# Kernel tuning notes

Measured on AMD Instinct MI355X. Metric: run time of the kernel, lower is better.

## Reference

```python
import jax, jax.numpy as jnp
import numpy as np

N, E, B = 20000, 200000, 16
ND, ED, GD, HD, DOF = 64, 32, 32, 128, 6
PI = 3.14159265358979

def _hat(v):
    x, y, z = v[..., 0], v[..., 1], v[..., 2]
    O = jnp.zeros_like(x)
    return jnp.stack([jnp.stack([O, -z, y], -1),
                      jnp.stack([z, O, -x], -1),
                      jnp.stack([-y, x, O], -1)], -2)

def _so3_exp(phi):
    th2 = jnp.sum(phi * phi, -1, keepdims=True)
    th = jnp.sqrt(th2 + 1e-12)
    a = jnp.where(th < 1e-4, 1.0 - th2 / 6.0, jnp.sin(th) / th)
    b = jnp.where(th < 1e-4, 0.5 - th2 / 24.0, (1.0 - jnp.cos(th)) / th2)
    K = _hat(phi)
    I = jnp.eye(3, dtype=phi.dtype)
    return I + a[..., None] * K + b[..., None] * (K @ K)

def _se3_exp(rho, phi):
    # returns (R, t) of Exp([rho, phi]) with rotation part phi
    th2 = jnp.sum(phi * phi, -1, keepdims=True)
    th = jnp.sqrt(th2 + 1e-12)
    a = jnp.where(th < 1e-4, 1.0 - th2 / 6.0, jnp.sin(th) / th)
    b = jnp.where(th < 1e-4, 0.5 - th2 / 24.0, (1.0 - jnp.cos(th)) / th2)
    c = jnp.where(th < 1e-4, 1.0 / 6.0 - th2 / 120.0, (th - jnp.sin(th)) / (th2 * th))
    K = _hat(phi)
    KK = K @ K
    I = jnp.eye(3, dtype=phi.dtype)
    R = I + a[..., None] * K + b[..., None] * KK
    V = I + b[..., None] * K + c[..., None] * KK
    t = jnp.einsum('nij,nj->ni', V, rho)
    return R, t

def _comp(Ra, ta, Rb, tb):
    return Ra @ Rb, jnp.einsum('nij,nj->ni', Ra, tb) + ta

def _inv(R, t):
    Rt = jnp.swapaxes(R, -1, -2)
    return Rt, -jnp.einsum('nij,nj->ni', Rt, t)

def _vec(R, t):
    # flattened [R | t] 3x4 -> 12
    return jnp.concatenate([R, t[..., None]], -1).reshape(R.shape[0], 12)

def setup_inputs() -> dict:
    key = jax.random.key(0)
    ks = jax.random.split(key, 16)
    T_R = _so3_exp(0.5 * jax.random.normal(ks[0], (N, 3)))
    Tij_R = _so3_exp(0.5 * jax.random.normal(ks[1], (E, 3)))
    return {
        'xfeat': jax.random.normal(ks[2], (N, ND), jnp.float32),
        'T_R': T_R.astype(jnp.float32),
        'T_t': jax.random.normal(ks[3], (N, 3), jnp.float32),
        'edge_feat': jax.random.normal(ks[4], (E, ED), jnp.float32),
        'Tij_R': Tij_R.astype(jnp.float32),
        'Tij_t': jax.random.normal(ks[5], (E, 3), jnp.float32),
        'u': jax.random.normal(ks[6], (B, GD), jnp.float32),
        'edge_index': jax.random.randint(ks[7], (2, E), 0, N),
        'batch': jnp.sort(jax.random.randint(ks[8], (N,), 0, B)),
        'W1': 0.05 * jax.random.normal(ks[9], (2 * ND + 12 + ED, HD), jnp.float32),
        'b1': jnp.zeros((HD,), jnp.float32),
        'W2': 0.05 * jax.random.normal(ks[10], (HD, HD), jnp.float32),
        'b2': jnp.zeros((HD,), jnp.float32),
        'W3': 0.05 * jax.random.normal(ks[11], (HD + GD + ND, HD), jnp.float32),
        'b3': jnp.zeros((HD,), jnp.float32),
        'W4': 0.05 * jax.random.normal(ks[12], (HD, ND + DOF), jnp.float32),
        'b4': jnp.zeros((ND + DOF,), jnp.float32),
    }

def reference(xfeat, T_R, T_t, edge_feat, Tij_R, Tij_t, u,
              edge_index, batch, W1, b1, W2, b2, W3, b3, W4, b4):
    n = xfeat.shape[0]
    i, j = edge_index[0], edge_index[1]
    xfi, xfj = xfeat[i], xfeat[j]
    Ri, ti = T_R[i], T_t[i]
    Rj, tj = T_R[j], T_t[j]
    # T_err_ij = Tj * Ti.inv() * Tij_hat.inv()
    Rii, tii = _inv(Ri, ti)
    Ra, ta = _comp(Rj, tj, Rii, tii)
    Rhi, thi = _inv(Tij_R, Tij_t)
    Reij, teij = _comp(Ra, ta, Rhi, thi)
    # T_err_ji = Ti * Tj.inv() * Tij_hat
    Rji_, tji_ = _inv(Rj, tj)
    Rb, tb = _comp(Ri, ti, Rji_, tji_)
    Reji, teji = _comp(Rb, tb, Tij_R, Tij_t)
    f_ij = jnp.concatenate([xfi, xfj, edge_feat, _vec(Reij, teij)], 1)
    f_ji = jnp.concatenate([xfj, xfi, edge_feat, _vec(Reji, teji)], 1)
    feats = jnp.concatenate([f_ij, f_ji], 0)          # [2E, 172]
    j_both = jnp.concatenate([j, i], 0)               # [2E]
    h = jax.nn.relu(feats @ W1 + b1)
    h = jax.nn.relu(h @ W2 + b2)                      # [2E, HD]
    sums = jax.ops.segment_sum(h, j_both, num_segments=n)
    cnt = jax.ops.segment_sum(jnp.ones((h.shape[0], 1), h.dtype), j_both, num_segments=n)
    aggr = sums / jnp.maximum(cnt, 1.0)               # scatter_mean
    g = jnp.concatenate([aggr, xfeat, u[batch]], 1)
    out = jax.nn.relu(g @ W3 + b3) @ W4 + b4
    xupd, tupd = out[:, :-DOF], out[:, -DOF:]
    rho, phi = tupd[:, :3], tupd[:, 3:]
    # SquashRot: bound rotation angle to pi via tanh
    th = jnp.linalg.norm(phi, axis=-1, keepdims=True)
    phi = phi * (PI * jnp.tanh(th / PI) / (th + 1e-8))
    Rd, td = _se3_exp(rho, phi)
    R_out, t_out = _comp(Rd, td, T_R, T_t)            # boxplus_left: Exp(d) * T
    xfeat_out = xfeat + xupd
    theta = jnp.linalg.norm(phi, axis=-1, keepdims=True)
    return jnp.concatenate([xfeat_out, R_out.reshape(n, 9), t_out, theta], -1)
```

## Files before the change

### kernel.cpp

```cpp
#include <hip/hip_runtime.h>
#include <math.h>

#define ND 64
#define ED 32
#define GD 32
#define HD 128
#define DOF 6
#define K1 172
#define K1PAD 192
#define KG 224
#define N4P 80
#define NOUT 70
#define OUTC 77
#define MT 128
#define FP 200
#define TD 32
#define GP 232
#define HP 136
#define OP 84
#define MAXD 96
#define PI_F 3.14159265358979f

typedef short short8 __attribute__((ext_vector_type(8)));
typedef float f32x4  __attribute__((ext_vector_type(4)));

__device__ __forceinline__ unsigned short f2b(float f) {
    unsigned int u = __float_as_uint(f);
    u += 0x7fffu + ((u >> 16) & 1u);
    return (unsigned short)(u >> 16);
}
__device__ __forceinline__ float b2f(unsigned short b) {
    return __uint_as_float(((unsigned int)b) << 16);
}

__device__ __forceinline__ void mul33_abt(const float* A, const float* B, float* C) {
#pragma unroll
    for (int r = 0; r < 3; r++)
#pragma unroll
        for (int c = 0; c < 3; c++)
            C[3*r+c] = A[3*r+0]*B[3*c+0] + A[3*r+1]*B[3*c+1] + A[3*r+2]*B[3*c+2];
}

__global__ void __launch_bounds__(256)
pack_w(const float* __restrict__ W1, const float* __restrict__ W2,
       const float* __restrict__ W3, const float* __restrict__ W4,
       unsigned short* __restrict__ W1b, unsigned short* __restrict__ W2b,
       unsigned short* __restrict__ W3b, unsigned short* __restrict__ W4b)
{
    int idx = blockIdx.x * 256 + threadIdx.x;
    if (idx < K1PAD * HD) {
        int k = idx >> 7, n = idx & 127;
        float v = (k < K1) ? W1[k * HD + n] : 0.f;
        int kc = k >> 5, kr = k & 31, q = kr >> 3, j = kr & 7;
        W1b[(((kc * 8 + (n >> 4)) * 4 + q) * 16 + (n & 15)) * 8 + j] = f2b(v);
        return;
    }
    idx -= K1PAD * HD;
    if (idx < HD * HD) {
        int k = idx >> 7, n = idx & 127;
        float v = W2[k * HD + n];
        int kc = k >> 5, kr = k & 31, q = kr >> 3, j = kr & 7;
        W2b[(((kc * 8 + (n >> 4)) * 4 + q) * 16 + (n & 15)) * 8 + j] = f2b(v);
        return;
    }
    idx -= HD * HD;
    if (idx < KG * HD) {
        int k = idx >> 7, n = idx & 127;
        int sk = (k < HD) ? ((k & 7) * 16 + (k >> 3)) : k;
        float v = W3[sk * HD + n];
        int kc = k >> 5, kr = k & 31, q = kr >> 3, j = kr & 7;
        W3b[(((kc * 8 + (n >> 4)) * 4 + q) * 16 + (n & 15)) * 8 + j] = f2b(v);
        return;
    }
    idx -= KG * HD;
    if (idx < HD * N4P) {
        int k = idx / N4P, n = idx % N4P;
        float v = (n < NOUT) ? W4[k * NOUT + n] : 0.f;
        int kc = k >> 5, kr = k & 31, q = kr >> 3, j = kr & 7;
        W4b[(((kc * 5 + (n >> 4)) * 4 + q) * 16 + (n & 15)) * 8 + j] = f2b(v);
    }
}

__global__ void __launch_bounds__(256)
build_csr(const int* __restrict__ edge_index, int* __restrict__ cnti,
          int* __restrict__ list, int E)
{
    int d = blockIdx.x * 256 + threadIdx.x;
    if (d >= 2 * E) return;
    const int tgt = (d < E) ? edge_index[E + d] : edge_index[d - E];
    const int slot = atomicAdd(&cnti[tgt], 1);
    if (slot < MAXD) list[(size_t)tgt * MAXD + slot] = d;
}

__global__ void __launch_bounds__(256, 3)
edge_kernel(const float* __restrict__ xfeat, const float* __restrict__ T_R,
            const float* __restrict__ T_t, const float* __restrict__ edge_feat,
            const float* __restrict__ Tij_R, const float* __restrict__ Tij_t,
            const int* __restrict__ edge_index,
            const unsigned short* __restrict__ W1b, const float* __restrict__ b1,
            const unsigned short* __restrict__ W2b, const float* __restrict__ b2,
            unsigned short* __restrict__ hbuf, int E)
{
    __shared__ unsigned short fbuf[MT * FP];
    const int tid = threadIdx.x;
    const int dir0 = blockIdx.x * MT;
    const int ndir = min(MT, 2 * E - dir0);

    {
        const int r = tid >> 1;
        const int half = tid & 1;
        const int drow = dir0 + r;
        int s1 = 0, s2 = 0, er = 0;
        if (r < ndir) {
            const bool fwd = (drow < E);
            er = fwd ? drow : drow - E;
            const int ni = edge_index[er];
            const int nj = edge_index[E + er];
            s1 = fwd ? ni : nj;
            s2 = fwd ? nj : ni;
        }
#pragma unroll
        for (int gg = 0; gg < 20; gg++) {
            const int c4 = (half * 20 + gg) * 4;
            float4 v;
            if (c4 < 64)        v = *(const float4*)&xfeat[s1 * ND + c4];
            else if (c4 < 128)  v = *(const float4*)&xfeat[s2 * ND + (c4 - 64)];
            else                v = *(const float4*)&edge_feat[er * ED + (c4 - 128)];
            ushort4 o; o.x = f2b(v.x); o.y = f2b(v.y); o.z = f2b(v.z); o.w = f2b(v.w);
            *(ushort4*)&fbuf[r * FP + c4] = o;
        }
    }
    if (tid < MT && tid < ndir) {
        const int dir = dir0 + tid;
        const bool fwd = (dir < E);
        const int e = fwd ? dir : dir - E;
        const int ni = edge_index[e];
        const int nj = edge_index[E + e];
        float Ri[9], Rj[9], TR[9], ti[3], tj[3], Tt[3];
#pragma unroll
        for (int q = 0; q < 9; q++) { Ri[q] = T_R[9*ni+q]; Rj[q] = T_R[9*nj+q]; TR[q] = Tij_R[9*e+q]; }
#pragma unroll
        for (int q = 0; q < 3; q++) { ti[q] = T_t[3*ni+q]; tj[q] = T_t[3*nj+q]; Tt[q] = Tij_t[3*e+q]; }
        float A[9];
        mul33_abt(Rj, Ri, A);
        float Re[9], te[3];
        if (fwd) {
            mul33_abt(A, TR, Re);
#pragma unroll
            for (int r = 0; r < 3; r++)
                te[r] = tj[r]
                      - (A[3*r+0]*ti[0] + A[3*r+1]*ti[1] + A[3*r+2]*ti[2])
                      - (Re[3*r+0]*Tt[0] + Re[3*r+1]*Tt[1] + Re[3*r+2]*Tt[2]);
        } else {
#pragma unroll
            for (int r = 0; r < 3; r++)
#pragma unroll
                for (int c = 0; c < 3; c++)
                    Re[3*r+c] = A[r]*TR[c] + A[3+r]*TR[3+c] + A[6+r]*TR[6+c];
            const float d0 = Tt[0]-tj[0], d1 = Tt[1]-tj[1], d2 = Tt[2]-tj[2];
#pragma unroll
            for (int r = 0; r < 3; r++)
                te[r] = ti[r] + A[r]*d0 + A[3+r]*d1 + A[6+r]*d2;
        }
        unsigned short* fr = &fbuf[tid * FP];
#pragma unroll
        for (int r = 0; r < 3; r++) {
            fr[160 + 4*r + 0] = f2b(Re[3*r+0]);
            fr[160 + 4*r + 1] = f2b(Re[3*r+1]);
            fr[160 + 4*r + 2] = f2b(Re[3*r+2]);
            fr[160 + 4*r + 3] = f2b(te[r]);
        }
#pragma unroll
        for (int c = 172; c < K1PAD; c++) fr[c] = 0;
    }
    __syncthreads();

    const int wv = tid >> 6;
    const int lane = tid & 63;
    const int nl = lane & 15;
    const int quad = lane >> 4;
    const int m0w = wv * 32;
    const int laneoff = quad * 128 + nl * 8;

    float bias1[8], bias2[8];
#pragma unroll
    for (int nt = 0; nt < 8; nt++) { bias1[nt] = b1[nt*16 + nl]; bias2[nt] = b2[nt*16 + nl]; }

    f32x4 acc[2][8];
#pragma unroll
    for (int rt = 0; rt < 2; rt++)
#pragma unroll
        for (int nt = 0; nt < 8; nt++) acc[rt][nt] = (f32x4)0.f;

#pragma unroll
    for (int kc = 0; kc < 6; kc++) {
        short8 a0 = *(const short8*)&fbuf[(m0w +  0 + nl) * FP + kc*32 + quad*8];
        short8 a1 = *(const short8*)&fbuf[(m0w + 16 + nl) * FP + kc*32 + quad*8];
#pragma unroll
        for (int nt = 0; nt < 8; nt++) {
            short8 b = *(const short8*)(W1b + (kc*8 + nt)*512 + laneoff);
            acc[0][nt] = __builtin_amdgcn_mfma_f32_16x16x32_bf16(a0, b, acc[0][nt], 0, 0, 0);
            acc[1][nt] = __builtin_amdgcn_mfma_f32_16x16x32_bf16(a1, b, acc[1][nt], 0, 0, 0);
        }
    }
#pragma unroll
    for (int rt = 0; rt < 2; rt++)
#pragma unroll
        for (int nt = 0; nt < 8; nt++) {
            const int col = nt*16 + nl;
#pragma unroll
            for (int r = 0; r < 4; r++) {
                const int row = m0w + rt*16 + quad*4 + r;
                fbuf[row * FP + col] = f2b(fmaxf(acc[rt][nt][r] + bias1[nt], 0.f));
            }
        }

#pragma unroll
    for (int rt = 0; rt < 2; rt++)
#pragma unroll
        for (int nt = 0; nt < 8; nt++) acc[rt][nt] = (f32x4)0.f;
#pragma unroll
    for (int kc = 0; kc < 4; kc++) {
        short8 a0 = *(const short8*)&fbuf[(m0w +  0 + nl) * FP + kc*32 + quad*8];
        short8 a1 = *(const short8*)&fbuf[(m0w + 16 + nl) * FP + kc*32 + quad*8];
#pragma unroll
        for (int nt = 0; nt < 8; nt++) {
            short8 b = *(const short8*)(W2b + (kc*8 + nt)*512 + laneoff);
            acc[0][nt] = __builtin_amdgcn_mfma_f32_16x16x32_bf16(a0, b, acc[0][nt], 0, 0, 0);
            acc[1][nt] = __builtin_amdgcn_mfma_f32_16x16x32_bf16(a1, b, acc[1][nt], 0, 0, 0);
        }
    }

#pragma unroll
    for (int rt = 0; rt < 2; rt++)
#pragma unroll
        for (int r = 0; r < 4; r++) {
            const int m = m0w + rt*16 + quad*4 + r;
            if (m < ndir) {
                short8 hv;
#pragma unroll
                for (int nt = 0; nt < 8; nt++)
                    hv[nt] = (short)f2b(fmaxf(acc[rt][nt][r] + bias2[nt], 0.f));
                *(short8*)(hbuf + (size_t)(dir0 + m) * HD + nl*8) = hv;
            }
        }
}

__global__ void __launch_bounds__(256)
node_kernel(const float* __restrict__ xfeat, const float* __restrict__ T_R,
            const float* __restrict__ T_t, const float* __restrict__ u,
            const int* __restrict__ batch,
            const unsigned short* __restrict__ W3b, const float* __restrict__ b3,
            const unsigned short* __restrict__ W4b, const float* __restrict__ b4,
            const unsigned short* __restrict__ hbuf, const int* __restrict__ list,
            const int* __restrict__ cnti,
            float* __restrict__ out, int Nn)
{
    __shared__ unsigned short gbuf[TD * GP];
    __shared__ unsigned short hid[TD * HP];
    __shared__ float obuf[TD * OP];
    const int tid = threadIdx.x;
    const int wv = tid >> 6, lane = tid & 63;
    const int n0 = blockIdx.x * TD;
    const int nn = min(TD, Nn - n0);

#pragma unroll 2
    for (int i = 0; i < 8; i++) {
        const int d = wv + 4*i;
        if (d < nn) {
            const int n = n0 + d;
            const int deg = cnti[n];
            const int degl = min(deg, MAXD);
            const float inv = 1.0f / (float)max(deg, 1);
            const int* lp = list + (size_t)n * MAXD;
            float a0 = 0.f, a1 = 0.f;
            int k = 0;
            for (; k + 2 <= degl; k += 2) {
                const int e0 = lp[k], e1 = lp[k+1];
                const unsigned int v0 = *(const unsigned int*)(hbuf + (size_t)e0 * HD + 2*lane);
                const unsigned int v1 = *(const unsigned int*)(hbuf + (size_t)e1 * HD + 2*lane);
                a0 += b2f((unsigned short)v0) + b2f((unsigned short)v1);
                a1 += b2f((unsigned short)(v0 >> 16)) + b2f((unsigned short)(v1 >> 16));
            }
            if (k < degl) {
                const unsigned int v0 = *(const unsigned int*)(hbuf + (size_t)lp[k] * HD + 2*lane);
                a0 += b2f((unsigned short)v0);
                a1 += b2f((unsigned short)(v0 >> 16));
            }
            const unsigned int pk = (unsigned int)f2b(a0 * inv) | ((unsigned int)f2b(a1 * inv) << 16);
            *(unsigned int*)&gbuf[d * GP + 2*lane] = pk;
        }
    }
    for (int idx = tid; idx < TD * 24; idx += 256) {
        const int d = idx / 24;
        if (d < nn) {
            const int n = n0 + d;
            const int c4 = (idx % 24) * 4;
            float4 v;
            if (c4 < 64) v = *(const float4*)&xfeat[(size_t)n * ND + c4];
            else         v = *(const float4*)&u[(size_t)batch[n] * GD + (c4 - 64)];
            ushort4 o; o.x = f2b(v.x); o.y = f2b(v.y); o.z = f2b(v.z); o.w = f2b(v.w);
            *(ushort4*)&gbuf[d * GP + 128 + c4] = o;
        }
    }
    __syncthreads();

    const int nl = lane & 15, quad = lane >> 4;
    const int laneoff = quad * 128 + nl * 8;

    f32x4 acc3[2][2];
#pragma unroll
    for (int mt = 0; mt < 2; mt++)
#pragma unroll
        for (int t = 0; t < 2; t++) acc3[mt][t] = (f32x4)0.f;
#pragma unroll
    for (int kc = 0; kc < 7; kc++) {
        short8 A0 = *(const short8*)&gbuf[( 0 + nl) * GP + kc*32 + quad*8];
        short8 A1 = *(const short8*)&gbuf[(16 + nl) * GP + kc*32 + quad*8];
#pragma unroll
        for (int t = 0; t < 2; t++) {
            const int nt = wv*2 + t;
            short8 B = *(const short8*)(W3b + (kc*8 + nt)*512 + laneoff);
            acc3[0][t] = __builtin_amdgcn_mfma_f32_16x16x32_bf16(A0, B, acc3[0][t], 0, 0, 0);
            acc3[1][t] = __builtin_amdgcn_mfma_f32_16x16x32_bf16(A1, B, acc3[1][t], 0, 0, 0);
        }
    }
#pragma unroll
    for (int t = 0; t < 2; t++) {
        const int col = (wv*2 + t)*16 + nl;
        const float bb = b3[col];
#pragma unroll
        for (int mt = 0; mt < 2; mt++)
#pragma unroll
            for (int r = 0; r < 4; r++)
                hid[(mt*16 + quad*4 + r) * HP + col] = f2b(fmaxf(acc3[mt][t][r] + bb, 0.f));
    }
    __syncthreads();

    f32x4 acc4[2][2];
#pragma unroll
    for (int mt = 0; mt < 2; mt++)
#pragma unroll
        for (int t = 0; t < 2; t++) acc4[mt][t] = (f32x4)0.f;
    const int nt1 = (wv == 0) ? 4 : -1;
#pragma unroll
    for (int kc = 0; kc < 4; kc++) {
        short8 A0 = *(const short8*)&hid[( 0 + nl) * HP + kc*32 + quad*8];
        short8 A1 = *(const short8*)&hid[(16 + nl) * HP + kc*32 + quad*8];
        short8 B0 = *(const short8*)(W4b + (kc*5 + wv)*512 + laneoff);
        acc4[0][0] = __builtin_amdgcn_mfma_f32_16x16x32_bf16(A0, B0, acc4[0][0], 0, 0, 0);
        acc4[1][0] = __builtin_amdgcn_mfma_f32_16x16x32_bf16(A1, B0, acc4[1][0], 0, 0, 0);
        if (nt1 >= 0) {
            short8 B1 = *(const short8*)(W4b + (kc*5 + nt1)*512 + laneoff);
            acc4[0][1] = __builtin_amdgcn_mfma_f32_16x16x32_bf16(A0, B1, acc4[0][1], 0, 0, 0);
            acc4[1][1] = __builtin_amdgcn_mfma_f32_16x16x32_bf16(A1, B1, acc4[1][1], 0, 0, 0);
        }
    }
    {
        const int col0 = wv*16 + nl;
        const float bb0 = (col0 < NOUT) ? b4[col0] : 0.f;
#pragma unroll
        for (int mt = 0; mt < 2; mt++)
#pragma unroll
            for (int r = 0; r < 4; r++)
                obuf[(mt*16 + quad*4 + r) * OP + col0] = acc4[mt][0][r] + bb0;
        if (nt1 >= 0) {
            const int col1 = nt1*16 + nl;
            const float bb1 = (col1 < NOUT) ? b4[col1] : 0.f;
#pragma unroll
            for (int mt = 0; mt < 2; mt++)
#pragma unroll
                for (int r = 0; r < 4; r++)
                    obuf[(mt*16 + quad*4 + r) * OP + col1] = acc4[mt][1][r] + bb1;
        }
    }
    __syncthreads();

    for (int idx = tid; idx < TD * ND; idx += 256) {
        const int d = idx >> 6, c = idx & 63;
        if (d < nn) {
            const int n = n0 + d;
            out[(size_t)n * OUTC + c] = xfeat[(size_t)n * ND + c] + obuf[d * OP + c];
        }
    }
    if (tid < nn) {
        const int n = n0 + tid;
        const float r0 = obuf[tid*OP + 64], r1 = obuf[tid*OP + 65], r2 = obuf[tid*OP + 66];
        float p0 = obuf[tid*OP + 67], p1 = obuf[tid*OP + 68], p2 = obuf[tid*OP + 69];
        const float th0 = sqrtf(p0*p0 + p1*p1 + p2*p2);
        const float s = PI_F * tanhf(th0 / PI_F) / (th0 + 1e-8f);
        p0 *= s; p1 *= s; p2 *= s;
        const float pp = p0*p0 + p1*p1 + p2*p2;
        const float th = sqrtf(pp + 1e-12f);
        float a, b, c;
        if (th < 1e-4f) { a = 1.f - pp/6.f; b = 0.5f - pp/24.f; c = 1.f/6.f - pp/120.f; }
        else { const float sn = sinf(th), cs = cosf(th); a = sn/th; b = (1.f-cs)/pp; c = (th-sn)/(pp*th); }
        float Rd[9], V[9];
        Rd[0]=1.f+b*(p0*p0-pp); Rd[1]=-a*p2+b*p0*p1; Rd[2]= a*p1+b*p0*p2;
        Rd[3]= a*p2+b*p1*p0;    Rd[4]=1.f+b*(p1*p1-pp); Rd[5]=-a*p0+b*p1*p2;
        Rd[6]=-a*p1+b*p2*p0;    Rd[7]= a*p0+b*p2*p1;  Rd[8]=1.f+b*(p2*p2-pp);
        V[0]=1.f+c*(p0*p0-pp);  V[1]=-b*p2+c*p0*p1;   V[2]= b*p1+c*p0*p2;
        V[3]= b*p2+c*p1*p0;     V[4]=1.f+c*(p1*p1-pp); V[5]=-b*p0+c*p1*p2;
        V[6]=-b*p1+c*p2*p0;     V[7]= b*p0+c*p2*p1;   V[8]=1.f+c*(p2*p2-pp);
        const float td0 = V[0]*r0 + V[1]*r1 + V[2]*r2;
        const float td1 = V[3]*r0 + V[4]*r1 + V[5]*r2;
        const float td2 = V[6]*r0 + V[7]*r1 + V[8]*r2;
        float TRn[9], Ttn[3];
#pragma unroll
        for (int q = 0; q < 9; q++) TRn[q] = T_R[9*n+q];
#pragma unroll
        for (int q = 0; q < 3; q++) Ttn[q] = T_t[3*n+q];
        float* o = out + (size_t)n * OUTC + 64;
#pragma unroll
        for (int r = 0; r < 3; r++)
#pragma unroll
            for (int cc = 0; cc < 3; cc++)
                o[3*r+cc] = Rd[3*r+0]*TRn[cc] + Rd[3*r+1]*TRn[3+cc] + Rd[3*r+2]*TRn[6+cc];
        o[9]  = Rd[0]*Ttn[0] + Rd[1]*Ttn[1] + Rd[2]*Ttn[2] + td0;
        o[10] = Rd[3]*Ttn[0] + Rd[4]*Ttn[1] + Rd[5]*Ttn[2] + td1;
        o[11] = Rd[6]*Ttn[0] + Rd[7]*Ttn[1] + Rd[8]*Ttn[2] + td2;
        o[12] = sqrtf(pp);
    }
}

extern "C" void kernel_launch(void* const* d_in, const int* in_sizes, int n_in,
                              void* d_out, int out_size, void* d_ws, size_t ws_size,
                              hipStream_t stream)
{
    const float* xfeat     = (const float*)d_in[0];
    const float* T_R       = (const float*)d_in[1];
    const float* T_t       = (const float*)d_in[2];
    const float* edge_feat = (const float*)d_in[3];
    const float* Tij_R     = (const float*)d_in[4];
    const float* Tij_t     = (const float*)d_in[5];
    const float* u         = (const float*)d_in[6];
    const int*   edge_index= (const int*)d_in[7];
    const int*   batch     = (const int*)d_in[8];
    const float* W1 = (const float*)d_in[9],  *b1 = (const float*)d_in[10];
    const float* W2 = (const float*)d_in[11], *b2 = (const float*)d_in[12];
    const float* W3 = (const float*)d_in[13], *b3 = (const float*)d_in[14];
    const float* W4 = (const float*)d_in[15], *b4 = (const float*)d_in[16];
    const int N = in_sizes[0] / ND;
    const int E = in_sizes[3] / ED;

    char* p = (char*)d_ws;
    unsigned short* W1b = (unsigned short*)p;  p += (size_t)K1PAD * HD * 2;
    unsigned short* W2b = (unsigned short*)p;  p += (size_t)HD * HD * 2;
    unsigned short* W3b = (unsigned short*)p;  p += (size_t)KG * HD * 2;
    unsigned short* W4b = (unsigned short*)p;  p += (size_t)HD * N4P * 2;
    unsigned short* hbuf = (unsigned short*)p; p += (size_t)2 * E * HD * 2;
    int* list = (int*)p;                       p += (size_t)N * MAXD * 4;
    int* cnti = (int*)p;

    hipMemsetAsync(cnti, 0, (size_t)N * 4, stream);
    const int packn = K1PAD*HD + HD*HD + KG*HD + HD*N4P;
    pack_w<<<(packn + 255) / 256, 256, 0, stream>>>(W1, W2, W3, W4, W1b, W2b, W3b, W4b);
    build_csr<<<(2 * E + 255) / 256, 256, 0, stream>>>(edge_index, cnti, list, E);

    const int eb = (2 * E + MT - 1) / MT;
    edge_kernel<<<eb, 256, 0, stream>>>(xfeat, T_R, T_t, edge_feat, Tij_R, Tij_t,
                                        edge_index, W1b, b1, W2b, b2, hbuf, E);
    const int nb = (N + TD - 1) / TD;
    node_kernel<<<nb, 256, 0, stream>>>(xfeat, T_R, T_t, u, batch, W3b, b3, W4b, b4,
                                        hbuf, list, cnti, (float*)d_out, N);
}
```

Baseline: 311.7 us.

## Precompute bf16 features and edge poses, load MFMA operands directly from global

```diff
diff --git a/kernel.cpp b/kernel.cpp
--- a/kernel.cpp
+++ b/kernel.cpp
@@ -13,8 +13,8 @@
 #define NOUT 70
 #define OUTC 77
 #define MT 128
-#define FP 200
-#define TD 32
+#define HP1 136
+#define TDN 16
 #define GP 232
 #define HP 136
 #define OP 84
@@ -32,7 +32,6 @@
 __device__ __forceinline__ float b2f(unsigned short b) {
     return __uint_as_float(((unsigned int)b) << 16);
 }
-
 __device__ __forceinline__ void mul33_abt(const float* A, const float* B, float* C) {
 #pragma unroll
     for (int r = 0; r < 3; r++)
@@ -42,10 +41,13 @@
 }
 
 __global__ void __launch_bounds__(256)
-pack_w(const float* __restrict__ W1, const float* __restrict__ W2,
-       const float* __restrict__ W3, const float* __restrict__ W4,
-       unsigned short* __restrict__ W1b, unsigned short* __restrict__ W2b,
-       unsigned short* __restrict__ W3b, unsigned short* __restrict__ W4b)
+prep(const float* __restrict__ W1, const float* __restrict__ W2,
+     const float* __restrict__ W3, const float* __restrict__ W4,
+     const float* __restrict__ xfeat, const float* __restrict__ edge_feat,
+     unsigned short* __restrict__ W1b, unsigned short* __restrict__ W2b,
+     unsigned short* __restrict__ W3b, unsigned short* __restrict__ W4b,
+     unsigned short* __restrict__ xb, unsigned short* __restrict__ eb,
+     int N, int E)
 {
     int idx = blockIdx.x * 256 + threadIdx.x;
     if (idx < K1PAD * HD) {
@@ -58,18 +60,16 @@
     idx -= K1PAD * HD;
     if (idx < HD * HD) {
         int k = idx >> 7, n = idx & 127;
-        float v = W2[k * HD + n];
         int kc = k >> 5, kr = k & 31, q = kr >> 3, j = kr & 7;
-        W2b[(((kc * 8 + (n >> 4)) * 4 + q) * 16 + (n & 15)) * 8 + j] = f2b(v);
+        W2b[(((kc * 8 + (n >> 4)) * 4 + q) * 16 + (n & 15)) * 8 + j] = f2b(W2[k * HD + n]);
         return;
     }
     idx -= HD * HD;
     if (idx < KG * HD) {
         int k = idx >> 7, n = idx & 127;
         int sk = (k < HD) ? ((k & 7) * 16 + (k >> 3)) : k;
-        float v = W3[sk * HD + n];
         int kc = k >> 5, kr = k & 31, q = kr >> 3, j = kr & 7;
-        W3b[(((kc * 8 + (n >> 4)) * 4 + q) * 16 + (n & 15)) * 8 + j] = f2b(v);
+        W3b[(((kc * 8 + (n >> 4)) * 4 + q) * 16 + (n & 15)) * 8 + j] = f2b(W3[sk * HD + n]);
         return;
     }
     idx -= KG * HD;
@@ -78,109 +78,122 @@
         float v = (n < NOUT) ? W4[k * NOUT + n] : 0.f;
         int kc = k >> 5, kr = k & 31, q = kr >> 3, j = kr & 7;
         W4b[(((kc * 5 + (n >> 4)) * 4 + q) * 16 + (n & 15)) * 8 + j] = f2b(v);
+        return;
+    }
+    idx -= HD * N4P;
+    const int nx4 = N * ND / 4;
+    if (idx < nx4) {
+        const float4 v = *(const float4*)&xfeat[idx * 4];
+        ushort4 o; o.x = f2b(v.x); o.y = f2b(v.y); o.z = f2b(v.z); o.w = f2b(v.w);
+        *(ushort4*)&xb[idx * 4] = o;
+        return;
+    }
+    idx -= nx4;
+    if (idx < E * ED / 4) {
+        const float4 v = *(const float4*)&edge_feat[idx * 4];
+        ushort4 o; o.x = f2b(v.x); o.y = f2b(v.y); o.z = f2b(v.z); o.w = f2b(v.w);
+        *(ushort4*)&eb[idx * 4] = o;
     }
 }
 
 __global__ void __launch_bounds__(256)
-build_csr(const int* __restrict__ edge_index, int* __restrict__ cnti,
-          int* __restrict__ list, int E)
+pose_csr(const float* __restrict__ T_R, const float* __restrict__ T_t,
+         const float* __restrict__ Tij_R, const float* __restrict__ Tij_t,
+         const int* __restrict__ edge_index,
+         unsigned short* __restrict__ poseb, int* __restrict__ cnti,
+         int* __restrict__ list, int E)
 {
-    int d = blockIdx.x * 256 + threadIdx.x;
-    if (d >= 2 * E) return;
-    const int tgt = (d < E) ? edge_index[E + d] : edge_index[d - E];
+    const int g = blockIdx.x * 256 + threadIdx.x;
+    if (g >= 2 * E) return;
+    const bool fwd = (g < E);
+    const int e = fwd ? g : g - E;
+    const int ni = edge_index[e];
+    const int nj = edge_index[E + e];
+    const int tgt = fwd ? nj : ni;
     const int slot = atomicAdd(&cnti[tgt], 1);
-    if (slot < MAXD) list[(size_t)tgt * MAXD + slot] = d;
+    if (slot < MAXD) list[(size_t)tgt * MAXD + slot] = g;
+
+    float Ri[9], Rj[9], TR[9], ti[3], tj[3], Tt[3];
+#pragma unroll
+    for (int q = 0; q < 9; q++) { Ri[q] = T_R[9*ni+q]; Rj[q] = T_R[9*nj+q]; TR[q] = Tij_R[9*e+q]; }
+#pragma unroll
+    for (int q = 0; q < 3; q++) { ti[q] = T_t[3*ni+q]; tj[q] = T_t[3*nj+q]; Tt[q] = Tij_t[3*e+q]; }
+    float A[9];
+    mul33_abt(Rj, Ri, A);
+    float Re[9], te[3];
+    if (fwd) {
+        mul33_abt(A, TR, Re);
+#pragma unroll
+        for (int r = 0; r < 3; r++)
+            te[r] = tj[r]
+                  - (A[3*r+0]*ti[0] + A[3*r+1]*ti[1] + A[3*r+2]*ti[2])
+                  - (Re[3*r+0]*Tt[0] + Re[3*r+1]*Tt[1] + Re[3*r+2]*Tt[2]);
+    } else {
+#pragma unroll
+        for (int r = 0; r < 3; r++)
+#pragma unroll
+            for (int c = 0; c < 3; c++)
+                Re[3*r+c] = A[r]*TR[c] + A[3+r]*TR[3+c] + A[6+r]*TR[6+c];
+        const float d0 = Tt[0]-tj[0], d1 = Tt[1]-tj[1], d2 = Tt[2]-tj[2];
+#pragma unroll
+        for (int r = 0; r < 3; r++)
+            te[r] = ti[r] + A[r]*d0 + A[3+r]*d1 + A[6+r]*d2;
+    }
+    short8 p0, p1;
+#pragma unroll
+    for (int r = 0; r < 2; r++) {
+        p0[4*r+0] = (short)f2b(Re[3*r+0]);
+        p0[4*r+1] = (short)f2b(Re[3*r+1]);
+        p0[4*r+2] = (short)f2b(Re[3*r+2]);
+        p0[4*r+3] = (short)f2b(te[r]);
+    }
+    p1[0] = (short)f2b(Re[6]); p1[1] = (short)f2b(Re[7]);
+    p1[2] = (short)f2b(Re[8]); p1[3] = (short)f2b(te[2]);
+    p1[4] = 0; p1[5] = 0; p1[6] = 0; p1[7] = 0;
+    *(short8*)(poseb + (size_t)g * 16) = p0;
+    *(short8*)(poseb + (size_t)g * 16 + 8) = p1;
 }
 
 __global__ void __launch_bounds__(256, 3)
-edge_kernel(const float* __restrict__ xfeat, const float* __restrict__ T_R,
-            const float* __restrict__ T_t, const float* __restrict__ edge_feat,
-            const float* __restrict__ Tij_R, const float* __restrict__ Tij_t,
-            const int* __restrict__ edge_index,
+edge_kernel(const unsigned short* __restrict__ xb, const unsigned short* __restrict__ eb,
+            const unsigned short* __restrict__ poseb, const int* __restrict__ edge_index,
             const unsigned short* __restrict__ W1b, const float* __restrict__ b1,
             const unsigned short* __restrict__ W2b, const float* __restrict__ b2,
             unsigned short* __restrict__ hbuf, int E)
 {
-    __shared__ unsigned short fbuf[MT * FP];
+    __shared__ unsigned short h1s[4 * 32 * HP1];
     const int tid = threadIdx.x;
-    const int dir0 = blockIdx.x * MT;
-    const int ndir = min(MT, 2 * E - dir0);
-
-    {
-        const int r = tid >> 1;
-        const int half = tid & 1;
-        const int drow = dir0 + r;
-        int s1 = 0, s2 = 0, er = 0;
-        if (r < ndir) {
-            const bool fwd = (drow < E);
-            er = fwd ? drow : drow - E;
-            const int ni = edge_index[er];
-            const int nj = edge_index[E + er];
-            s1 = fwd ? ni : nj;
-            s2 = fwd ? nj : ni;
-        }
-#pragma unroll
-        for (int gg = 0; gg < 20; gg++) {
-            const int c4 = (half * 20 + gg) * 4;
-            float4 v;
-            if (c4 < 64)        v = *(const float4*)&xfeat[s1 * ND + c4];
-            else if (c4 < 128)  v = *(const float4*)&xfeat[s2 * ND + (c4 - 64)];
-            else                v = *(const float4*)&edge_feat[er * ED + (c4 - 128)];
-            ushort4 o; o.x = f2b(v.x); o.y = f2b(v.y); o.z = f2b(v.z); o.w = f2b(v.w);
-            *(ushort4*)&fbuf[r * FP + c4] = o;
-        }
-    }
-    if (tid < MT && tid < ndir) {
-        const int dir = dir0 + tid;
-        const bool fwd = (dir < E);
-        const int e = fwd ? dir : dir - E;
+    const int wv = tid >> 6, lane = tid & 63;
+    const int nl = lane & 15, quad = lane >> 4;
+    const int D0 = blockIdx.x * MT + wv * 32;
+    const int laneoff = quad * 128 + nl * 8;
+    unsigned short* hw = h1s + wv * 32 * HP1;
+
+    int s1[2], s2[2], ee[2], gg[2];
+#pragma unroll
+    for (int rt = 0; rt < 2; rt++) {
+        int g = D0 + rt * 16 + nl;
+        if (g >= 2 * E) g = 2 * E - 1;
+        const bool fwd = (g < E);
+        const int e = fwd ? g : g - E;
         const int ni = edge_index[e];
         const int nj = edge_index[E + e];
-        float Ri[9], Rj[9], TR[9], ti[3], tj[3], Tt[3];
-#pragma unroll
-        for (int q = 0; q < 9; q++) { Ri[q] = T_R[9*ni+q]; Rj[q] = T_R[9*nj+q]; TR[q] = Tij_R[9*e+q]; }
-#pragma unroll
-        for (int q = 0; q < 3; q++) { ti[q] = T_t[3*ni+q]; tj[q] = T_t[3*nj+q]; Tt[q] = Tij_t[3*e+q]; }
-        float A[9];
-        mul33_abt(Rj, Ri, A);
-        float Re[9], te[3];
-        if (fwd) {
-            mul33_abt(A, TR, Re);
-#pragma unroll
-            for (int r = 0; r < 3; r++)
-                te[r] = tj[r]
-                      - (A[3*r+0]*ti[0] + A[3*r+1]*ti[1] + A[3*r+2]*ti[2])
-                      - (Re[3*r+0]*Tt[0] + Re[3*r+1]*Tt[1] + Re[3*r+2]*Tt[2]);
-        } else {
-#pragma unroll
-            for (int r = 0; r < 3; r++)
-#pragma unroll
-                for (int c = 0; c < 3; c++)
-                    Re[3*r+c] = A[r]*TR[c] + A[3+r]*TR[3+c] + A[6+r]*TR[6+c];
-            const float d0 = Tt[0]-tj[0], d1 = Tt[1]-tj[1], d2 = Tt[2]-tj[2];
-#pragma unroll
-            for (int r = 0; r < 3; r++)
-                te[r] = ti[r] + A[r]*d0 + A[3+r]*d1 + A[6+r]*d2;
-        }
-        unsigned short* fr = &fbuf[tid * FP];
-#pragma unroll
-        for (int r = 0; r < 3; r++) {
-            fr[160 + 4*r + 0] = f2b(Re[3*r+0]);
-            fr[160 + 4*r + 1] = f2b(Re[3*r+1]);
-            fr[160 + 4*r + 2] = f2b(Re[3*r+2]);
-            fr[160 + 4*r + 3] = f2b(te[r]);
-        }
-#pragma unroll
-        for (int c = 172; c < K1PAD; c++) fr[c] = 0;
-    }
-    __syncthreads();
-
-    const int wv = tid >> 6;
-    const int lane = tid & 63;
-    const int nl = lane & 15;
-    const int quad = lane >> 4;
-    const int m0w = wv * 32;
-    const int laneoff = quad * 128 + nl * 8;
+        s1[rt] = fwd ? ni : nj;
+        s2[rt] = fwd ? nj : ni;
+        ee[rt] = e; gg[rt] = g;
+    }
+
+    short8 a[2][6];
+#pragma unroll
+    for (int rt = 0; rt < 2; rt++) {
+        a[rt][0] = *(const short8*)(xb + (size_t)s1[rt] * ND + quad * 8);
+        a[rt][1] = *(const short8*)(xb + (size_t)s1[rt] * ND + 32 + quad * 8);
+        a[rt][2] = *(const short8*)(xb + (size_t)s2[rt] * ND + quad * 8);
+        a[rt][3] = *(const short8*)(xb + (size_t)s2[rt] * ND + 32 + quad * 8);
+        a[rt][4] = *(const short8*)(eb + (size_t)ee[rt] * ED + quad * 8);
+        a[rt][5] = (quad < 2) ? *(const short8*)(poseb + (size_t)gg[rt] * 16 + quad * 8)
+                              : (short8)(short)0;
+    }
 
     float bias1[8], bias2[8];
 #pragma unroll
@@ -194,26 +207,24 @@
 
 #pragma unroll
     for (int kc = 0; kc < 6; kc++) {
-        short8 a0 = *(const short8*)&fbuf[(m0w +  0 + nl) * FP + kc*32 + quad*8];
-        short8 a1 = *(const short8*)&fbuf[(m0w + 16 + nl) * FP + kc*32 + quad*8];
 #pragma unroll
         for (int nt = 0; nt < 8; nt++) {
             short8 b = *(const short8*)(W1b + (kc*8 + nt)*512 + laneoff);
-            acc[0][nt] = __builtin_amdgcn_mfma_f32_16x16x32_bf16(a0, b, acc[0][nt], 0, 0, 0);
-            acc[1][nt] = __builtin_amdgcn_mfma_f32_16x16x32_bf16(a1, b, acc[1][nt], 0, 0, 0);
-        }
-    }
+            acc[0][nt] = __builtin_amdgcn_mfma_f32_16x16x32_bf16(a[0][kc], b, acc[0][nt], 0, 0, 0);
+            acc[1][nt] = __builtin_amdgcn_mfma_f32_16x16x32_bf16(a[1][kc], b, acc[1][nt], 0, 0, 0);
+        }
+    }
+
 #pragma unroll
     for (int rt = 0; rt < 2; rt++)
 #pragma unroll
         for (int nt = 0; nt < 8; nt++) {
             const int col = nt*16 + nl;
 #pragma unroll
-            for (int r = 0; r < 4; r++) {
-                const int row = m0w + rt*16 + quad*4 + r;
-                fbuf[row * FP + col] = f2b(fmaxf(acc[rt][nt][r] + bias1[nt], 0.f));
-            }
-        }
+            for (int r = 0; r < 4; r++)
+                hw[(rt*16 + quad*4 + r) * HP1 + col] = f2b(fmaxf(acc[rt][nt][r] + bias1[nt], 0.f));
+        }
+    asm volatile("s_waitcnt lgkmcnt(0)" ::: "memory");
 
 #pragma unroll
     for (int rt = 0; rt < 2; rt++)
@@ -221,8 +232,8 @@
         for (int nt = 0; nt < 8; nt++) acc[rt][nt] = (f32x4)0.f;
 #pragma unroll
     for (int kc = 0; kc < 4; kc++) {
-        short8 a0 = *(const short8*)&fbuf[(m0w +  0 + nl) * FP + kc*32 + quad*8];
-        short8 a1 = *(const short8*)&fbuf[(m0w + 16 + nl) * FP + kc*32 + quad*8];
+        short8 a0 = *(const short8*)&hw[( 0 + nl) * HP1 + kc*32 + quad*8];
+        short8 a1 = *(const short8*)&hw[(16 + nl) * HP1 + kc*32 + quad*8];
 #pragma unroll
         for (int nt = 0; nt < 8; nt++) {
             short8 b = *(const short8*)(W2b + (kc*8 + nt)*512 + laneoff);
@@ -235,13 +246,13 @@
     for (int rt = 0; rt < 2; rt++)
 #pragma unroll
         for (int r = 0; r < 4; r++) {
-            const int m = m0w + rt*16 + quad*4 + r;
-            if (m < ndir) {
+            const int g2 = D0 + rt*16 + quad*4 + r;
+            if (g2 < 2 * E) {
                 short8 hv;
 #pragma unroll
                 for (int nt = 0; nt < 8; nt++)
                     hv[nt] = (short)f2b(fmaxf(acc[rt][nt][r] + bias2[nt], 0.f));
-                *(short8*)(hbuf + (size_t)(dir0 + m) * HD + nl*8) = hv;
+                *(short8*)(hbuf + (size_t)g2 * HD + nl*8) = hv;
             }
         }
 }
@@ -256,16 +267,16 @@
             const int* __restrict__ cnti,
             float* __restrict__ out, int Nn)
 {
-    __shared__ unsigned short gbuf[TD * GP];
-    __shared__ unsigned short hid[TD * HP];
-    __shared__ float obuf[TD * OP];
+    __shared__ unsigned short gbuf[TDN * GP];
+    __shared__ unsigned short hid[TDN * HP];
+    __shared__ float obuf[TDN * OP];
     const int tid = threadIdx.x;
     const int wv = tid >> 6, lane = tid & 63;
-    const int n0 = blockIdx.x * TD;
-    const int nn = min(TD, Nn - n0);
-
-#pragma unroll 2
-    for (int i = 0; i < 8; i++) {
+    const int n0 = blockIdx.x * TDN;
+    const int nn = min(TDN, Nn - n0);
+
+#pragma unroll
+    for (int i = 0; i < 4; i++) {
         const int d = wv + 4*i;
         if (d < nn) {
             const int n = n0 + d;
@@ -291,7 +302,7 @@
             *(unsigned int*)&gbuf[d * GP + 2*lane] = pk;
         }
     }
-    for (int idx = tid; idx < TD * 24; idx += 256) {
+    for (int idx = tid; idx < TDN * 24; idx += 256) {
         const int d = idx / 24;
         if (d < nn) {
             const int n = n0 + d;
@@ -308,21 +319,15 @@
     const int nl = lane & 15, quad = lane >> 4;
     const int laneoff = quad * 128 + nl * 8;
 
-    f32x4 acc3[2][2];
-#pragma unroll
-    for (int mt = 0; mt < 2; mt++)
-#pragma unroll
-        for (int t = 0; t < 2; t++) acc3[mt][t] = (f32x4)0.f;
+    f32x4 acc3[2];
+    acc3[0] = (f32x4)0.f; acc3[1] = (f32x4)0.f;
 #pragma unroll
     for (int kc = 0; kc < 7; kc++) {
-        short8 A0 = *(const short8*)&gbuf[( 0 + nl) * GP + kc*32 + quad*8];
-        short8 A1 = *(const short8*)&gbuf[(16 + nl) * GP + kc*32 + quad*8];
+        short8 A0 = *(const short8*)&gbuf[nl * GP + kc*32 + quad*8];
 #pragma unroll
         for (int t = 0; t < 2; t++) {
-            const int nt = wv*2 + t;
-            short8 B = *(const short8*)(W3b + (kc*8 + nt)*512 + laneoff);
-            acc3[0][t] = __builtin_amdgcn_mfma_f32_16x16x32_bf16(A0, B, acc3[0][t], 0, 0, 0);
-            acc3[1][t] = __builtin_amdgcn_mfma_f32_16x16x32_bf16(A1, B, acc3[1][t], 0, 0, 0);
+            short8 B = *(const short8*)(W3b + (kc*8 + wv*2 + t)*512 + laneoff);
+            acc3[t] = __builtin_amdgcn_mfma_f32_16x16x32_bf16(A0, B, acc3[t], 0, 0, 0);
         }
     }
 #pragma unroll
@@ -330,53 +335,41 @@
         const int col = (wv*2 + t)*16 + nl;
         const float bb = b3[col];
 #pragma unroll
-        for (int mt = 0; mt < 2; mt++)
-#pragma unroll
-            for (int r = 0; r < 4; r++)
-                hid[(mt*16 + quad*4 + r) * HP + col] = f2b(fmaxf(acc3[mt][t][r] + bb, 0.f));
+        for (int r = 0; r < 4; r++)
+            hid[(quad*4 + r) * HP + col] = f2b(fmaxf(acc3[t][r] + bb, 0.f));
     }
     __syncthreads();
 
-    f32x4 acc4[2][2];
-#pragma unroll
-    for (int mt = 0; mt < 2; mt++)
-#pragma unroll
-        for (int t = 0; t < 2; t++) acc4[mt][t] = (f32x4)0.f;
+    f32x4 acc4[2];
+    acc4[0] = (f32x4)0.f; acc4[1] = (f32x4)0.f;
     const int nt1 = (wv == 0) ? 4 : -1;
 #pragma unroll
     for (int kc = 0; kc < 4; kc++) {
-        short8 A0 = *(const short8*)&hid[( 0 + nl) * HP + kc*32 + quad*8];
-        short8 A1 = *(const short8*)&hid[(16 + nl) * HP + kc*32 + quad*8];
+        short8 A0 = *(const short8*)&hid[nl * HP + kc*32 + quad*8];
         short8 B0 = *(const short8*)(W4b + (kc*5 + wv)*512 + laneoff);
-        acc4[0][0] = __builtin_amdgcn_mfma_f32_16x16x32_bf16(A0, B0, acc4[0][0], 0, 0, 0);
-        acc4[1][0] = __builtin_amdgcn_mfma_f32_16x16x32_bf16(A1, B0, acc4[1][0], 0, 0, 0);
+        acc4[0] = __builtin_amdgcn_mfma_f32_16x16x32_bf16(A0, B0, acc4[0], 0, 0, 0);
         if (nt1 >= 0) {
             short8 B1 = *(const short8*)(W4b + (kc*5 + nt1)*512 + laneoff);
-            acc4[0][1] = __builtin_amdgcn_mfma_f32_16x16x32_bf16(A0, B1, acc4[0][1], 0, 0, 0);
-            acc4[1][1] = __builtin_amdgcn_mfma_f32_16x16x32_bf16(A1, B1, acc4[1][1], 0, 0, 0);
+            acc4[1] = __builtin_amdgcn_mfma_f32_16x16x32_bf16(A0, B1, acc4[1], 0, 0, 0);
         }
     }
     {
         const int col0 = wv*16 + nl;
         const float bb0 = (col0 < NOUT) ? b4[col0] : 0.f;
 #pragma unroll
-        for (int mt = 0; mt < 2; mt++)
-#pragma unroll
-            for (int r = 0; r < 4; r++)
-                obuf[(mt*16 + quad*4 + r) * OP + col0] = acc4[mt][0][r] + bb0;
+        for (int r = 0; r < 4; r++)
+            obuf[(quad*4 + r) * OP + col0] = acc4[0][r] + bb0;
         if (nt1 >= 0) {
             const int col1 = nt1*16 + nl;
             const float bb1 = (col1 < NOUT) ? b4[col1] : 0.f;
 #pragma unroll
-            for (int mt = 0; mt < 2; mt++)
-#pragma unroll
-                for (int r = 0; r < 4; r++)
-                    obuf[(mt*16 + quad*4 + r) * OP + col1] = acc4[mt][1][r] + bb1;
+            for (int r = 0; r < 4; r++)
+                obuf[(quad*4 + r) * OP + col1] = acc4[1][r] + bb1;
         }
     }
     __syncthreads();
 
-    for (int idx = tid; idx < TD * ND; idx += 256) {
+    for (int idx = tid; idx < TDN * ND; idx += 256) {
         const int d = idx >> 6, c = idx & 63;
         if (d < nn) {
             const int n = n0 + d;
@@ -444,23 +437,27 @@
     const int E = in_sizes[3] / ED;
 
     char* p = (char*)d_ws;
-    unsigned short* W1b = (unsigned short*)p;  p += (size_t)K1PAD * HD * 2;
-    unsigned short* W2b = (unsigned short*)p;  p += (size_t)HD * HD * 2;
-    unsigned short* W3b = (unsigned short*)p;  p += (size_t)KG * HD * 2;
-    unsigned short* W4b = (unsigned short*)p;  p += (size_t)HD * N4P * 2;
-    unsigned short* hbuf = (unsigned short*)p; p += (size_t)2 * E * HD * 2;
-    int* list = (int*)p;                       p += (size_t)N * MAXD * 4;
+    unsigned short* W1b = (unsigned short*)p;   p += (size_t)K1PAD * HD * 2;
+    unsigned short* W2b = (unsigned short*)p;   p += (size_t)HD * HD * 2;
+    unsigned short* W3b = (unsigned short*)p;   p += (size_t)KG * HD * 2;
+    unsigned short* W4b = (unsigned short*)p;   p += (size_t)HD * N4P * 2;
+    unsigned short* xb  = (unsigned short*)p;   p += (size_t)N * ND * 2;
+    unsigned short* ebf = (unsigned short*)p;   p += (size_t)E * ED * 2;
+    unsigned short* poseb = (unsigned short*)p; p += (size_t)2 * E * 16 * 2;
+    unsigned short* hbuf = (unsigned short*)p;  p += (size_t)2 * E * HD * 2;
+    int* list = (int*)p;                        p += (size_t)N * MAXD * 4;
     int* cnti = (int*)p;
 
     hipMemsetAsync(cnti, 0, (size_t)N * 4, stream);
-    const int packn = K1PAD*HD + HD*HD + KG*HD + HD*N4P;
-    pack_w<<<(packn + 255) / 256, 256, 0, stream>>>(W1, W2, W3, W4, W1b, W2b, W3b, W4b);
-    build_csr<<<(2 * E + 255) / 256, 256, 0, stream>>>(edge_index, cnti, list, E);
-
-    const int eb = (2 * E + MT - 1) / MT;
-    edge_kernel<<<eb, 256, 0, stream>>>(xfeat, T_R, T_t, edge_feat, Tij_R, Tij_t,
-                                        edge_index, W1b, b1, W2b, b2, hbuf, E);
-    const int nb = (N + TD - 1) / TD;
+    const int prepn = K1PAD*HD + HD*HD + KG*HD + HD*N4P + N*ND/4 + E*ED/4;
+    prep<<<(prepn + 255) / 256, 256, 0, stream>>>(W1, W2, W3, W4, xfeat, edge_feat,
+                                                  W1b, W2b, W3b, W4b, xb, ebf, N, E);
+    pose_csr<<<(2*E + 255) / 256, 256, 0, stream>>>(T_R, T_t, Tij_R, Tij_t, edge_index,
+                                                    poseb, cnti, list, E);
+    const int ebk = (2 * E + MT - 1) / MT;
+    edge_kernel<<<ebk, 256, 0, stream>>>(xb, ebf, poseb, edge_index,
+                                         W1b, b1, W2b, b2, hbuf, E);
+    const int nb = (N + TDN - 1) / TDN;
     node_kernel<<<nb, 256, 0, stream>>>(xfeat, T_R, T_t, u, batch, W3b, b3, W4b, b4,
                                         hbuf, list, cnti, (float*)d_out, N);
 }
```

New measurement: 295.8 us. 5.1% less time.
